# Performance work log

Hardware: AMD Instinct MI355X
Metric: run time of the kernel (lower is better)

Reference implementation:

```python
import jax, jax.numpy as jnp
import numpy as np

EPS = 1.0  # args.eps
N, D, H = 2097152, 2, 4

_PARAM_SPECS = [
    ("w_xin", (H, D)), ("b_xin", (H,)),
    ("w_xp1", (H, H)), ("b_xp1", (H,)),
    ("w_xp2", (H, H)), ("b_xp2", (H,)),
    ("w_xl1", (H, D)), ("b_xl1", (H,)),
    ("w_xl2", (H, H)), ("b_xl2", (H,)),
    ("w_xl3", (H, H)), ("b_xl3", (H,)),
    ("w_xlo", (1, H)), ("b_xlo", (1,)),
    ("w_cp1", (H, H)),  # PositiveLinear, no bias
    ("w_cp2", (H, H)),
    ("w_cpo", (1, H)),
    ("w_cp1m", (H, H)), ("b_cp1m", (H,)),
    ("w_cp2m", (H, H)), ("b_cp2m", (H,)),
    ("w_cpom", (H, H)), ("b_cpom", (H,)),
    ("w_clin", (H, D)),  # no bias
    ("w_cl1", (H, D)),
    ("w_cl2", (H, D)),
    ("w_clo", (1, D)),
    ("w_clinm", (D, D)), ("b_clinm", (D,)),
    ("w_cl1m", (D, H)), ("b_cl1m", (D,)),
    ("w_cl2m", (D, H)), ("b_cl2m", (D,)),
    ("w_clom", (D, H)), ("b_clom", (D,)),
]

def setup_inputs() -> dict:
    key = jax.random.key(0)
    k_x, k_xs, k_p = jax.random.split(key, 3)
    inp = {
        "x": jax.random.normal(k_x, (N, D), dtype=jnp.float32),
        "x_star": jax.random.normal(k_xs, (N, D), dtype=jnp.float32),
    }
    pkeys = jax.random.split(k_p, len(_PARAM_SPECS))
    for (name, shape), k in zip(_PARAM_SPECS, pkeys):
        if name.startswith("b_"):
            inp[name] = jnp.zeros(shape, dtype=jnp.float32)  # zeros bias init
        else:
            fan_in = shape[1]
            std = np.sqrt(2.0 / fan_in).astype(np.float32)  # kaiming normal
            inp[name] = jax.random.normal(k, shape, dtype=jnp.float32) * std
    return inp

def _lin(x, W, b=None):
    y = x @ W.T
    return y + b if b is not None else y

def _plin(x, W):
    # PositiveLinear reparam: W>=0 -> W + exp(-eps); W<0 -> exp(W - eps)
    Wr = jnp.where(W >= 0, W + jnp.exp(jnp.float32(-EPS)), jnp.exp(W - EPS))
    return x @ Wr.T

def reference(x, x_star,
              w_xin, b_xin, w_xp1, b_xp1, w_xp2, b_xp2,
              w_xl1, b_xl1, w_xl2, b_xl2, w_xl3, b_xl3, w_xlo, b_xlo,
              w_cp1, w_cp2, w_cpo,
              w_cp1m, b_cp1m, w_cp2m, b_cp2m, w_cpom, b_cpom,
              w_clin, w_cl1, w_cl2, w_clo,
              w_clinm, b_clinm, w_cl1m, b_cl1m, w_cl2m, b_cl2m, w_clom, b_clom):
    sp = jax.nn.softplus
    x0, x0s = x, x_star
    xs = sp(_lin(x0, w_xl1, b_xl1) + _lin(x0s * _lin(x0, w_clinm, b_clinm), w_clin))
    xh = sp(_lin(x0, w_xin, b_xin))
    xs = sp(_lin(xh, w_xl2, b_xl2)
            + _plin(xs * sp(_lin(xh, w_cp1m, b_cp1m)), w_cp1)
            + _lin(x0s * _lin(xh, w_cl1m, b_cl1m), w_cl1))
    xh = sp(_lin(xh, w_xp1, b_xp1))
    xs = sp(_lin(xh, w_xl3, b_xl3)
            + _plin(xs * sp(_lin(xh, w_cp2m, b_cp2m)), w_cp2)
            + _lin(x0s * _lin(xh, w_cl2m, b_cl2m), w_cl2))
    xh = sp(_lin(xh, w_xp2, b_xp2))
    out = sp(_lin(xh, w_xlo, b_xlo)
             + _plin(xs * sp(_lin(xh, w_cpom, b_cpom)), w_cpo)
             + _lin(x0s * _lin(xh, w_clom, b_clom), w_clo))
    return out  # [N, 1]
```

## Files before the change

kernel.cpp:

```cpp
#include <hip/hip_runtime.h>


#define NR 2
#define L2Ef 1.4426950408889634f
#define LN2f 0.6931471805599453f

__device__ __forceinline__ float sp2(float y) {
    float e = __builtin_amdgcn_exp2f(-fabsf(y));
    float l = __builtin_amdgcn_logf(1.0f + e);
    return fmaxf(y, 0.0f) + l;
}

__device__ __forceinline__ float posw(float w) {
    return (w >= 0.0f) ? (w + 0.36787944117144233f) : __expf(w - 1.0f);
}


__global__ __launch_bounds__(256)
void prep_kernel(
    const float* __restrict__ w_xin,  const float* __restrict__ b_xin,
    const float* __restrict__ w_xp1,  const float* __restrict__ b_xp1,
    const float* __restrict__ w_xp2,  const float* __restrict__ b_xp2,
    const float* __restrict__ w_xl1,  const float* __restrict__ b_xl1,
    const float* __restrict__ w_xl2,  const float* __restrict__ b_xl2,
    const float* __restrict__ w_xl3,  const float* __restrict__ b_xl3,
    const float* __restrict__ w_xlo,  const float* __restrict__ b_xlo,
    const float* __restrict__ w_cp1,  const float* __restrict__ w_cp2,
    const float* __restrict__ w_cpo,
    const float* __restrict__ w_cp1m, const float* __restrict__ b_cp1m,
    const float* __restrict__ w_cp2m, const float* __restrict__ b_cp2m,
    const float* __restrict__ w_cpom, const float* __restrict__ b_cpom,
    const float* __restrict__ w_clin, const float* __restrict__ w_cl1,
    const float* __restrict__ w_cl2,  const float* __restrict__ w_clo,
    const float* __restrict__ w_clinm,const float* __restrict__ b_clinm,
    const float* __restrict__ w_cl1m, const float* __restrict__ b_cl1m,
    const float* __restrict__ w_cl2m, const float* __restrict__ b_cl2m,
    const float* __restrict__ w_clom, const float* __restrict__ b_clom,
    float* __restrict__ wb)
{
    const int t = threadIdx.x;
#define CPY(dst, src, cnt)    if (t < (cnt)) wb[(dst)+t] = src[t];
#define SCL(dst, src, cnt, s) if (t < (cnt)) wb[(dst)+t] = (s) * src[t];
#define PW(dst, src, cnt)     if (t < (cnt)) wb[(dst)+t] = LN2f * posw(src[t]);
    SCL(0,   w_xl1,  8, L2Ef)
    SCL(8,   b_xl1,  4, L2Ef)
    SCL(12,  w_clin, 8, L2Ef)
    CPY(20,  w_clinm,4)
    CPY(24,  b_clinm,2)
    SCL(26,  w_xin,  8, L2Ef)
    SCL(34,  b_xin,  4, L2Ef)
    CPY(38,  w_cp1m,16)
    SCL(54,  b_cp1m, 4, L2Ef)
    SCL(58,  w_cl1m, 8, LN2f)
    CPY(66,  b_cl1m, 2)
    CPY(68,  w_xl2, 16)
    SCL(84,  b_xl2,  4, L2Ef)
    PW (88,  w_cp1, 16)
    SCL(104, w_cl1,  8, L2Ef)
    CPY(112, w_xp1, 16)
    SCL(128, b_xp1,  4, L2Ef)
    CPY(132, w_cp2m,16)
    SCL(148, b_cp2m, 4, L2Ef)
    SCL(152, w_cl2m, 8, LN2f)
    CPY(160, b_cl2m, 2)
    CPY(162, w_xl3, 16)
    SCL(178, b_xl3,  4, L2Ef)
    PW (182, w_cp2, 16)
    SCL(198, w_cl2,  8, L2Ef)
    CPY(206, w_xp2, 16)
    SCL(222, b_xp2,  4, L2Ef)
    CPY(226, w_cpom,16)
    SCL(242, b_cpom, 4, L2Ef)
    SCL(246, w_clom, 8, LN2f)
    CPY(254, b_clom, 2)
    CPY(256, w_xlo,  4)
    SCL(260, b_xlo,  1, L2Ef)
    PW (261, w_cpo,  4)
    SCL(265, w_clo,  2, L2Ef)
#undef CPY
#undef SCL
#undef PW
}

__device__ __forceinline__ void mid_stage(
    const float* __restrict__ wb,
    float xs[NR][4], float xh[NR][4], const float XS0[NR][2])
{
    float v[NR][4];
    #pragma unroll
    for (int h = 0; h < 4; ++h) {
        float w0 = wb[h*4+0], w1 = wb[h*4+1], w2 = wb[h*4+2], w3 = wb[h*4+3];
        float b  = wb[16+h];
        #pragma unroll
        for (int r = 0; r < NR; ++r) {
            float m = sp2(fmaf(w0, xh[r][0], fmaf(w1, xh[r][1], fmaf(w2, xh[r][2], fmaf(w3, xh[r][3], b)))));
            v[r][h] = xs[r][h] * m;
        }
    }
    float u[NR][2];
    #pragma unroll
    for (int d = 0; d < 2; ++d) {
        float w0 = wb[20+d*4+0], w1 = wb[20+d*4+1], w2 = wb[20+d*4+2], w3 = wb[20+d*4+3];
        float b  = wb[28+d];
        #pragma unroll
        for (int r = 0; r < NR; ++r) {
            float t = fmaf(w0, xh[r][0], fmaf(w1, xh[r][1], fmaf(w2, xh[r][2], fmaf(w3, xh[r][3], b))));
            u[r][d] = XS0[r][d] * t;
        }
    }
    float ns[NR][4], nh[NR][4];
    #pragma unroll
    for (int h = 0; h < 4; ++h) {
        float a0 = wb[30+h*4+0], a1 = wb[30+h*4+1], a2 = wb[30+h*4+2], a3 = wb[30+h*4+3];
        float ab = wb[46+h];
        float p0 = wb[50+h*4+0], p1 = wb[50+h*4+1], p2 = wb[50+h*4+2], p3 = wb[50+h*4+3];
        float c0 = wb[66+h*2+0], c1 = wb[66+h*2+1];
        #pragma unroll
        for (int r = 0; r < NR; ++r) {
            float t = fmaf(a0, xh[r][0], fmaf(a1, xh[r][1], fmaf(a2, xh[r][2], fmaf(a3, xh[r][3], ab))));
            t = fmaf(p0, v[r][0], fmaf(p1, v[r][1], fmaf(p2, v[r][2], fmaf(p3, v[r][3], t))));
            t = fmaf(c0, u[r][0], fmaf(c1, u[r][1], t));
            ns[r][h] = sp2(t);
        }
    }
    #pragma unroll
    for (int h = 0; h < 4; ++h) {
        float w0 = wb[74+h*4+0], w1 = wb[74+h*4+1], w2 = wb[74+h*4+2], w3 = wb[74+h*4+3];
        float b  = wb[90+h];
        #pragma unroll
        for (int r = 0; r < NR; ++r)
            nh[r][h] = sp2(fmaf(w0, xh[r][0], fmaf(w1, xh[r][1], fmaf(w2, xh[r][2], fmaf(w3, xh[r][3], b)))));
    }
    #pragma unroll
    for (int r = 0; r < NR; ++r)
        #pragma unroll
        for (int h = 0; h < 4; ++h) { xs[r][h] = ns[r][h]; xh[r][h] = nh[r][h]; }
}

__global__ __launch_bounds__(256, 4)
void dissip_main(const float* __restrict__ x, const float* __restrict__ xst,
                 const float* __restrict__ wb, float* __restrict__ out, int n)
{
    const int tid = blockIdx.x * blockDim.x + threadIdx.x;
    const int r0  = tid * NR;
    if (r0 >= n) return;
    const bool full = (r0 + NR <= n);

    float X0[NR][2], XS0[NR][2];
    if (full) {
        const float4 xa = *(const float4*)(x   + (size_t)r0 * 2);
        const float4 sa = *(const float4*)(xst + (size_t)r0 * 2);
        X0[0][0]=xa.x;  X0[0][1]=xa.y;  X0[1][0]=xa.z;  X0[1][1]=xa.w;
        XS0[0][0]=sa.x; XS0[0][1]=sa.y; XS0[1][0]=sa.z; XS0[1][1]=sa.w;
    } else {
        #pragma unroll
        for (int r = 0; r < NR; ++r) {
            int row = r0 + r;
            if (row < n) {
                X0[r][0]  = x[(size_t)row*2];   X0[r][1]  = x[(size_t)row*2+1];
                XS0[r][0] = xst[(size_t)row*2]; XS0[r][1] = xst[(size_t)row*2+1];
            } else { X0[r][0]=X0[r][1]=XS0[r][0]=XS0[r][1]=0.0f; }
        }
    }

    float xs[NR][4], xh[NR][4];

    float tcl[NR][2];
    {
        float m00=wb[20], m01=wb[21], m10=wb[22], m11=wb[23], c0=wb[24], c1=wb[25];
        #pragma unroll
        for (int r = 0; r < NR; ++r) {
            tcl[r][0] = XS0[r][0] * fmaf(m00, X0[r][0], fmaf(m01, X0[r][1], c0));
            tcl[r][1] = XS0[r][1] * fmaf(m10, X0[r][0], fmaf(m11, X0[r][1], c1));
        }
    }
    #pragma unroll
    for (int h = 0; h < 4; ++h) {
        float a0 = wb[h*2+0], a1 = wb[h*2+1], ab = wb[8+h];
        float c0 = wb[12+h*2+0], c1 = wb[12+h*2+1];
        #pragma unroll
        for (int r = 0; r < NR; ++r) {
            float a = fmaf(a0, X0[r][0], fmaf(a1, X0[r][1], ab));
            a = fmaf(c0, tcl[r][0], fmaf(c1, tcl[r][1], a));
            xs[r][h] = sp2(a);
        }
    }
    #pragma unroll
    for (int h = 0; h < 4; ++h) {
        float w0 = wb[26+h*2+0], w1 = wb[26+h*2+1], b = wb[34+h];
        #pragma unroll
        for (int r = 0; r < NR; ++r)
            xh[r][h] = sp2(fmaf(w0, X0[r][0], fmaf(w1, X0[r][1], b)));
    }

    mid_stage(wb + 38,  xs, xh, XS0);
    mid_stage(wb + 132, xs, xh, XS0);

    float o[NR];
    {
        const float* ob = wb + 226;
        float vv[NR][4];
        #pragma unroll
        for (int h = 0; h < 4; ++h) {
            float w0 = ob[h*4+0], w1 = ob[h*4+1], w2 = ob[h*4+2], w3 = ob[h*4+3];
            float b  = ob[16+h];
            #pragma unroll
            for (int r = 0; r < NR; ++r) {
                float m = sp2(fmaf(w0, xh[r][0], fmaf(w1, xh[r][1], fmaf(w2, xh[r][2], fmaf(w3, xh[r][3], b)))));
                vv[r][h] = xs[r][h] * m;
            }
        }
        float uu[NR][2];
        #pragma unroll
        for (int d = 0; d < 2; ++d) {
            float w0 = ob[20+d*4+0], w1 = ob[20+d*4+1], w2 = ob[20+d*4+2], w3 = ob[20+d*4+3];
            float b  = ob[28+d];
            #pragma unroll
            for (int r = 0; r < NR; ++r) {
                float t = fmaf(w0, xh[r][0], fmaf(w1, xh[r][1], fmaf(w2, xh[r][2], fmaf(w3, xh[r][3], b))));
                uu[r][d] = XS0[r][d] * t;
            }
        }
        float l0 = ob[30], l1 = ob[31], l2 = ob[32], l3 = ob[33], lb = ob[34];
        float p0 = ob[35], p1 = ob[36], p2 = ob[37], p3 = ob[38];
        float c0 = ob[39], c1 = ob[40];
        #pragma unroll
        for (int r = 0; r < NR; ++r) {
            float t = fmaf(l0, xh[r][0], fmaf(l1, xh[r][1], fmaf(l2, xh[r][2], fmaf(l3, xh[r][3], lb))));
            t = fmaf(p0, vv[r][0], fmaf(p1, vv[r][1], fmaf(p2, vv[r][2], fmaf(p3, vv[r][3], t))));
            t = fmaf(c0, uu[r][0], fmaf(c1, uu[r][1], t));
            o[r] = LN2f * sp2(t);
        }
    }

    if (full) {
        *(float2*)(out + r0) = make_float2(o[0], o[1]);
    } else {
        #pragma unroll
        for (int r = 0; r < NR; ++r)
            if (r0 + r < n) out[r0 + r] = o[r];
    }
}

extern "C" void kernel_launch(void* const* d_in, const int* in_sizes, int n_in,
                              void* d_out, int out_size, void* d_ws, size_t ws_size,
                              hipStream_t stream) {
    const float* p[37];
    for (int i = 0; i < 37; ++i) p[i] = (const float*)d_in[i];
    float* wb = (float*)d_ws;
    const int n = in_sizes[0] / 2;

    prep_kernel<<<dim3(1), dim3(256), 0, stream>>>(
        p[2],  p[3],  p[4],  p[5],  p[6],  p[7],
        p[8],  p[9],  p[10], p[11], p[12], p[13],
        p[14], p[15],
        p[16], p[17], p[18],
        p[19], p[20], p[21], p[22], p[23], p[24],
        p[25], p[26], p[27], p[28],
        p[29], p[30], p[31], p[32], p[33], p[34],
        p[35], p[36],
        wb);

    const int threads = 256;
    const int rows_per_block = threads * NR;
    const int blocks = (n + rows_per_block - 1) / rows_per_block;
    dissip_main<<<dim3(blocks), dim3(threads), 0, stream>>>(
        p[0], p[1], wb, (float*)d_out, n);
}
```

Before: 180.6 us.

## Pack two rows into float2 vectors for packed FMA and split prep across blocks

Rewrites the main MLP kernel so each thread keeps its two rows in 2-wide float vectors, letting the compiler emit packed FP32 FMA/mul/max instructions (v_pk_fma_f32) instead of scalar ones. The transcendental softplus parts stay scalar. The weight-prep kernel is also split into 35 single-wave blocks, one per parameter segment, so all loads are issued in parallel instead of serially in one block. The aim is to cut VALU instruction count in this compute-bound kernel, at the risk of extra register moves for the packed layout.

```diff
diff --git a/kernel.cpp b/kernel.cpp
--- a/kernel.cpp
+++ b/kernel.cpp
@@ -1,22 +1,30 @@
 #include <hip/hip_runtime.h>
 
+
+typedef float v2f __attribute__((ext_vector_type(2)));
 
 #define NR 2
 #define L2Ef 1.4426950408889634f
 #define LN2f 0.6931471805599453f
 
-__device__ __forceinline__ float sp2(float y) {
-    float e = __builtin_amdgcn_exp2f(-fabsf(y));
-    float l = __builtin_amdgcn_logf(1.0f + e);
-    return fmaxf(y, 0.0f) + l;
-}
-
+__device__ __forceinline__ v2f vsplat(float s) { v2f r; r.x = s; r.y = s; return r; }
+__device__ __forceinline__ v2f vfma(float w, v2f x, v2f a) {
+    return __builtin_elementwise_fma(vsplat(w), x, a);
+}
+__device__ __forceinline__ v2f sp2v(v2f y) {
+    v2f e, l;
+    e.x = __builtin_amdgcn_exp2f(-fabsf(y.x));
+    e.y = __builtin_amdgcn_exp2f(-fabsf(y.y));
+    l.x = __builtin_amdgcn_logf(1.0f + e.x);
+    l.y = __builtin_amdgcn_logf(1.0f + e.y);
+    return __builtin_elementwise_max(y, vsplat(0.0f)) + l;
+}
 __device__ __forceinline__ float posw(float w) {
     return (w >= 0.0f) ? (w + 0.36787944117144233f) : __expf(w - 1.0f);
 }
 
 
-__global__ __launch_bounds__(256)
+__global__ __launch_bounds__(64)
 void prep_kernel(
     const float* __restrict__ w_xin,  const float* __restrict__ b_xin,
     const float* __restrict__ w_xp1,  const float* __restrict__ b_xp1,
@@ -39,102 +47,83 @@
     float* __restrict__ wb)
 {
     const int t = threadIdx.x;
-#define CPY(dst, src, cnt)    if (t < (cnt)) wb[(dst)+t] = src[t];
-#define SCL(dst, src, cnt, s) if (t < (cnt)) wb[(dst)+t] = (s) * src[t];
-#define PW(dst, src, cnt)     if (t < (cnt)) wb[(dst)+t] = LN2f * posw(src[t]);
-    SCL(0,   w_xl1,  8, L2Ef)
-    SCL(8,   b_xl1,  4, L2Ef)
-    SCL(12,  w_clin, 8, L2Ef)
-    CPY(20,  w_clinm,4)
-    CPY(24,  b_clinm,2)
-    SCL(26,  w_xin,  8, L2Ef)
-    SCL(34,  b_xin,  4, L2Ef)
-    CPY(38,  w_cp1m,16)
-    SCL(54,  b_cp1m, 4, L2Ef)
-    SCL(58,  w_cl1m, 8, LN2f)
-    CPY(66,  b_cl1m, 2)
-    CPY(68,  w_xl2, 16)
-    SCL(84,  b_xl2,  4, L2Ef)
-    PW (88,  w_cp1, 16)
-    SCL(104, w_cl1,  8, L2Ef)
-    CPY(112, w_xp1, 16)
-    SCL(128, b_xp1,  4, L2Ef)
-    CPY(132, w_cp2m,16)
-    SCL(148, b_cp2m, 4, L2Ef)
-    SCL(152, w_cl2m, 8, LN2f)
-    CPY(160, b_cl2m, 2)
-    CPY(162, w_xl3, 16)
-    SCL(178, b_xl3,  4, L2Ef)
-    PW (182, w_cp2, 16)
-    SCL(198, w_cl2,  8, L2Ef)
-    CPY(206, w_xp2, 16)
-    SCL(222, b_xp2,  4, L2Ef)
-    CPY(226, w_cpom,16)
-    SCL(242, b_cpom, 4, L2Ef)
-    SCL(246, w_clom, 8, LN2f)
-    CPY(254, b_clom, 2)
-    CPY(256, w_xlo,  4)
-    SCL(260, b_xlo,  1, L2Ef)
-    PW (261, w_cpo,  4)
-    SCL(265, w_clo,  2, L2Ef)
-#undef CPY
-#undef SCL
-#undef PW
-}
-
-__device__ __forceinline__ void mid_stage(
-    const float* __restrict__ wb,
-    float xs[NR][4], float xh[NR][4], const float XS0[NR][2])
+#define SEG(i, dst, src, cnt, EXPR) \
+    case i: if (t < (cnt)) { float s_ = (src)[t]; wb[(dst)+t] = (EXPR); } break;
+    switch (blockIdx.x) {
+    SEG(0,  0,   w_xl1,  8,  L2Ef*s_)
+    SEG(1,  8,   b_xl1,  4,  L2Ef*s_)
+    SEG(2,  12,  w_clin, 8,  L2Ef*s_)
+    SEG(3,  20,  w_clinm,4,  s_)
+    SEG(4,  24,  b_clinm,2,  s_)
+    SEG(5,  26,  w_xin,  8,  L2Ef*s_)
+    SEG(6,  34,  b_xin,  4,  L2Ef*s_)
+    SEG(7,  38,  w_cp1m, 16, s_)
+    SEG(8,  54,  b_cp1m, 4,  L2Ef*s_)
+    SEG(9,  58,  w_cl1m, 8,  LN2f*s_)
+    SEG(10, 66,  b_cl1m, 2,  s_)
+    SEG(11, 68,  w_xl2,  16, s_)
+    SEG(12, 84,  b_xl2,  4,  L2Ef*s_)
+    SEG(13, 88,  w_cp1,  16, LN2f*posw(s_))
+    SEG(14, 104, w_cl1,  8,  L2Ef*s_)
+    SEG(15, 112, w_xp1,  16, s_)
+    SEG(16, 128, b_xp1,  4,  L2Ef*s_)
+    SEG(17, 132, w_cp2m, 16, s_)
+    SEG(18, 148, b_cp2m, 4,  L2Ef*s_)
+    SEG(19, 152, w_cl2m, 8,  LN2f*s_)
+    SEG(20, 160, b_cl2m, 2,  s_)
+    SEG(21, 162, w_xl3,  16, s_)
+    SEG(22, 178, b_xl3,  4,  L2Ef*s_)
+    SEG(23, 182, w_cp2,  16, LN2f*posw(s_))
+    SEG(24, 198, w_cl2,  8,  L2Ef*s_)
+    SEG(25, 206, w_xp2,  16, s_)
+    SEG(26, 222, b_xp2,  4,  L2Ef*s_)
+    SEG(27, 226, w_cpom, 16, s_)
+    SEG(28, 242, b_cpom, 4,  L2Ef*s_)
+    SEG(29, 246, w_clom, 8,  LN2f*s_)
+    SEG(30, 254, b_clom, 2,  s_)
+    SEG(31, 256, w_xlo,  4,  s_)
+    SEG(32, 260, b_xlo,  1,  L2Ef*s_)
+    SEG(33, 261, w_cpo,  4,  LN2f*posw(s_))
+    SEG(34, 265, w_clo,  2,  L2Ef*s_)
+    }
+#undef SEG
+}
+
+__device__ __forceinline__ void mid_stage(const float* __restrict__ wb,
+                                          v2f xs[4], v2f xh[4], const v2f XS0[2])
 {
-    float v[NR][4];
-    #pragma unroll
-    for (int h = 0; h < 4; ++h) {
-        float w0 = wb[h*4+0], w1 = wb[h*4+1], w2 = wb[h*4+2], w3 = wb[h*4+3];
-        float b  = wb[16+h];
-        #pragma unroll
-        for (int r = 0; r < NR; ++r) {
-            float m = sp2(fmaf(w0, xh[r][0], fmaf(w1, xh[r][1], fmaf(w2, xh[r][2], fmaf(w3, xh[r][3], b)))));
-            v[r][h] = xs[r][h] * m;
-        }
-    }
-    float u[NR][2];
+    v2f v[4];
+    #pragma unroll
+    for (int h = 0; h < 4; ++h) {
+        v2f t = vfma(wb[h*4+0], xh[0], vfma(wb[h*4+1], xh[1],
+                vfma(wb[h*4+2], xh[2], vfma(wb[h*4+3], xh[3], vsplat(wb[16+h])))));
+        v[h] = xs[h] * sp2v(t);
+    }
+    v2f u[2];
     #pragma unroll
     for (int d = 0; d < 2; ++d) {
-        float w0 = wb[20+d*4+0], w1 = wb[20+d*4+1], w2 = wb[20+d*4+2], w3 = wb[20+d*4+3];
-        float b  = wb[28+d];
-        #pragma unroll
-        for (int r = 0; r < NR; ++r) {
-            float t = fmaf(w0, xh[r][0], fmaf(w1, xh[r][1], fmaf(w2, xh[r][2], fmaf(w3, xh[r][3], b))));
-            u[r][d] = XS0[r][d] * t;
-        }
-    }
-    float ns[NR][4], nh[NR][4];
-    #pragma unroll
-    for (int h = 0; h < 4; ++h) {
-        float a0 = wb[30+h*4+0], a1 = wb[30+h*4+1], a2 = wb[30+h*4+2], a3 = wb[30+h*4+3];
-        float ab = wb[46+h];
-        float p0 = wb[50+h*4+0], p1 = wb[50+h*4+1], p2 = wb[50+h*4+2], p3 = wb[50+h*4+3];
-        float c0 = wb[66+h*2+0], c1 = wb[66+h*2+1];
-        #pragma unroll
-        for (int r = 0; r < NR; ++r) {
-            float t = fmaf(a0, xh[r][0], fmaf(a1, xh[r][1], fmaf(a2, xh[r][2], fmaf(a3, xh[r][3], ab))));
-            t = fmaf(p0, v[r][0], fmaf(p1, v[r][1], fmaf(p2, v[r][2], fmaf(p3, v[r][3], t))));
-            t = fmaf(c0, u[r][0], fmaf(c1, u[r][1], t));
-            ns[r][h] = sp2(t);
-        }
-    }
-    #pragma unroll
-    for (int h = 0; h < 4; ++h) {
-        float w0 = wb[74+h*4+0], w1 = wb[74+h*4+1], w2 = wb[74+h*4+2], w3 = wb[74+h*4+3];
-        float b  = wb[90+h];
-        #pragma unroll
-        for (int r = 0; r < NR; ++r)
-            nh[r][h] = sp2(fmaf(w0, xh[r][0], fmaf(w1, xh[r][1], fmaf(w2, xh[r][2], fmaf(w3, xh[r][3], b)))));
-    }
-    #pragma unroll
-    for (int r = 0; r < NR; ++r)
-        #pragma unroll
-        for (int h = 0; h < 4; ++h) { xs[r][h] = ns[r][h]; xh[r][h] = nh[r][h]; }
+        v2f t = vfma(wb[20+d*4+0], xh[0], vfma(wb[20+d*4+1], xh[1],
+                vfma(wb[20+d*4+2], xh[2], vfma(wb[20+d*4+3], xh[3], vsplat(wb[28+d])))));
+        u[d] = XS0[d] * t;
+    }
+    v2f ns[4], nh[4];
+    #pragma unroll
+    for (int h = 0; h < 4; ++h) {
+        v2f t = vfma(wb[30+h*4+0], xh[0], vfma(wb[30+h*4+1], xh[1],
+                vfma(wb[30+h*4+2], xh[2], vfma(wb[30+h*4+3], xh[3], vsplat(wb[46+h])))));
+        t = vfma(wb[50+h*4+0], v[0], vfma(wb[50+h*4+1], v[1],
+            vfma(wb[50+h*4+2], v[2], vfma(wb[50+h*4+3], v[3], t))));
+        t = vfma(wb[66+h*2+0], u[0], vfma(wb[66+h*2+1], u[1], t));
+        ns[h] = sp2v(t);
+    }
+    #pragma unroll
+    for (int h = 0; h < 4; ++h) {
+        v2f t = vfma(wb[74+h*4+0], xh[0], vfma(wb[74+h*4+1], xh[1],
+                vfma(wb[74+h*4+2], xh[2], vfma(wb[74+h*4+3], xh[3], vsplat(wb[90+h])))));
+        nh[h] = sp2v(t);
+    }
+    #pragma unroll
+    for (int h = 0; h < 4; ++h) { xs[h] = ns[h]; xh[h] = nh[h]; }
 }
 
 __global__ __launch_bounds__(256, 4)
@@ -146,99 +135,63 @@
     if (r0 >= n) return;
     const bool full = (r0 + NR <= n);
 
-    float X0[NR][2], XS0[NR][2];
+    v2f X0[2], XS0[2];
     if (full) {
         const float4 xa = *(const float4*)(x   + (size_t)r0 * 2);
         const float4 sa = *(const float4*)(xst + (size_t)r0 * 2);
-        X0[0][0]=xa.x;  X0[0][1]=xa.y;  X0[1][0]=xa.z;  X0[1][1]=xa.w;
-        XS0[0][0]=sa.x; XS0[0][1]=sa.y; XS0[1][0]=sa.z; XS0[1][1]=sa.w;
+        X0[0].x = xa.x;  X0[0].y = xa.z;  X0[1].x = xa.y;  X0[1].y = xa.w;
+        XS0[0].x = sa.x; XS0[0].y = sa.z; XS0[1].x = sa.y; XS0[1].y = sa.w;
     } else {
-        #pragma unroll
-        for (int r = 0; r < NR; ++r) {
-            int row = r0 + r;
-            if (row < n) {
-                X0[r][0]  = x[(size_t)row*2];   X0[r][1]  = x[(size_t)row*2+1];
-                XS0[r][0] = xst[(size_t)row*2]; XS0[r][1] = xst[(size_t)row*2+1];
-            } else { X0[r][0]=X0[r][1]=XS0[r][0]=XS0[r][1]=0.0f; }
-        }
-    }
-
-    float xs[NR][4], xh[NR][4];
-
-    float tcl[NR][2];
-    {
-        float m00=wb[20], m01=wb[21], m10=wb[22], m11=wb[23], c0=wb[24], c1=wb[25];
-        #pragma unroll
-        for (int r = 0; r < NR; ++r) {
-            tcl[r][0] = XS0[r][0] * fmaf(m00, X0[r][0], fmaf(m01, X0[r][1], c0));
-            tcl[r][1] = XS0[r][1] * fmaf(m10, X0[r][0], fmaf(m11, X0[r][1], c1));
-        }
-    }
-    #pragma unroll
-    for (int h = 0; h < 4; ++h) {
-        float a0 = wb[h*2+0], a1 = wb[h*2+1], ab = wb[8+h];
-        float c0 = wb[12+h*2+0], c1 = wb[12+h*2+1];
-        #pragma unroll
-        for (int r = 0; r < NR; ++r) {
-            float a = fmaf(a0, X0[r][0], fmaf(a1, X0[r][1], ab));
-            a = fmaf(c0, tcl[r][0], fmaf(c1, tcl[r][1], a));
-            xs[r][h] = sp2(a);
-        }
-    }
-    #pragma unroll
-    for (int h = 0; h < 4; ++h) {
-        float w0 = wb[26+h*2+0], w1 = wb[26+h*2+1], b = wb[34+h];
-        #pragma unroll
-        for (int r = 0; r < NR; ++r)
-            xh[r][h] = sp2(fmaf(w0, X0[r][0], fmaf(w1, X0[r][1], b)));
-    }
+        X0[0] = vsplat(0.0f); X0[1] = vsplat(0.0f);
+        XS0[0] = vsplat(0.0f); XS0[1] = vsplat(0.0f);
+        X0[0].x  = x[(size_t)r0*2];   X0[1].x  = x[(size_t)r0*2+1];
+        XS0[0].x = xst[(size_t)r0*2]; XS0[1].x = xst[(size_t)r0*2+1];
+    }
+
+    v2f xs[4], xh[4];
+
+    v2f tcl[2];
+    tcl[0] = XS0[0] * vfma(wb[20], X0[0], vfma(wb[21], X0[1], vsplat(wb[24])));
+    tcl[1] = XS0[1] * vfma(wb[22], X0[0], vfma(wb[23], X0[1], vsplat(wb[25])));
+    #pragma unroll
+    for (int h = 0; h < 4; ++h) {
+        v2f a = vfma(wb[h*2+0], X0[0], vfma(wb[h*2+1], X0[1], vsplat(wb[8+h])));
+        a = vfma(wb[12+h*2+0], tcl[0], vfma(wb[12+h*2+1], tcl[1], a));
+        xs[h] = sp2v(a);
+    }
+    #pragma unroll
+    for (int h = 0; h < 4; ++h)
+        xh[h] = sp2v(vfma(wb[26+h*2+0], X0[0], vfma(wb[26+h*2+1], X0[1], vsplat(wb[34+h]))));
 
     mid_stage(wb + 38,  xs, xh, XS0);
     mid_stage(wb + 132, xs, xh, XS0);
 
-    float o[NR];
-    {
-        const float* ob = wb + 226;
-        float vv[NR][4];
-        #pragma unroll
-        for (int h = 0; h < 4; ++h) {
-            float w0 = ob[h*4+0], w1 = ob[h*4+1], w2 = ob[h*4+2], w3 = ob[h*4+3];
-            float b  = ob[16+h];
-            #pragma unroll
-            for (int r = 0; r < NR; ++r) {
-                float m = sp2(fmaf(w0, xh[r][0], fmaf(w1, xh[r][1], fmaf(w2, xh[r][2], fmaf(w3, xh[r][3], b)))));
-                vv[r][h] = xs[r][h] * m;
-            }
-        }
-        float uu[NR][2];
-        #pragma unroll
-        for (int d = 0; d < 2; ++d) {
-            float w0 = ob[20+d*4+0], w1 = ob[20+d*4+1], w2 = ob[20+d*4+2], w3 = ob[20+d*4+3];
-            float b  = ob[28+d];
-            #pragma unroll
-            for (int r = 0; r < NR; ++r) {
-                float t = fmaf(w0, xh[r][0], fmaf(w1, xh[r][1], fmaf(w2, xh[r][2], fmaf(w3, xh[r][3], b))));
-                uu[r][d] = XS0[r][d] * t;
-            }
-        }
-        float l0 = ob[30], l1 = ob[31], l2 = ob[32], l3 = ob[33], lb = ob[34];
-        float p0 = ob[35], p1 = ob[36], p2 = ob[37], p3 = ob[38];
-        float c0 = ob[39], c1 = ob[40];
-        #pragma unroll
-        for (int r = 0; r < NR; ++r) {
-            float t = fmaf(l0, xh[r][0], fmaf(l1, xh[r][1], fmaf(l2, xh[r][2], fmaf(l3, xh[r][3], lb))));
-            t = fmaf(p0, vv[r][0], fmaf(p1, vv[r][1], fmaf(p2, vv[r][2], fmaf(p3, vv[r][3], t))));
-            t = fmaf(c0, uu[r][0], fmaf(c1, uu[r][1], t));
-            o[r] = LN2f * sp2(t);
-        }
-    }
+    const float* ob = wb + 226;
+    v2f vv[4];
+    #pragma unroll
+    for (int h = 0; h < 4; ++h) {
+        v2f t = vfma(ob[h*4+0], xh[0], vfma(ob[h*4+1], xh[1],
+                vfma(ob[h*4+2], xh[2], vfma(ob[h*4+3], xh[3], vsplat(ob[16+h])))));
+        vv[h] = xs[h] * sp2v(t);
+    }
+    v2f uu[2];
+    #pragma unroll
+    for (int d = 0; d < 2; ++d) {
+        v2f t = vfma(ob[20+d*4+0], xh[0], vfma(ob[20+d*4+1], xh[1],
+                vfma(ob[20+d*4+2], xh[2], vfma(ob[20+d*4+3], xh[3], vsplat(ob[28+d])))));
+        uu[d] = XS0[d] * t;
+    }
+    v2f t = vfma(ob[30], xh[0], vfma(ob[31], xh[1],
+            vfma(ob[32], xh[2], vfma(ob[33], xh[3], vsplat(ob[34])))));
+    t = vfma(ob[35], vv[0], vfma(ob[36], vv[1],
+        vfma(ob[37], vv[2], vfma(ob[38], vv[3], t))));
+    t = vfma(ob[39], uu[0], vfma(ob[40], uu[1], t));
+    v2f o = vsplat(LN2f) * sp2v(t);
 
     if (full) {
-        *(float2*)(out + r0) = make_float2(o[0], o[1]);
+        *(v2f*)(out + r0) = o;
     } else {
-        #pragma unroll
-        for (int r = 0; r < NR; ++r)
-            if (r0 + r < n) out[r0 + r] = o[r];
+        out[r0] = o.x;
     }
 }
 
@@ -250,7 +203,7 @@
     float* wb = (float*)d_ws;
     const int n = in_sizes[0] / 2;
 
-    prep_kernel<<<dim3(1), dim3(256), 0, stream>>>(
+    prep_kernel<<<dim3(35), dim3(64), 0, stream>>>(
         p[2],  p[3],  p[4],  p[5],  p[6],  p[7],
         p[8],  p[9],  p[10], p[11], p[12], p[13],
         p[14], p[15],
```

Result: faster. 161.8 us (-10.4%).
